# Performance work log

Measured on AMD Instinct MI355X. Metric: run time of the kernel, lower is better.

Reference implementation:

```python
import jax, jax.numpy as jnp
import numpy as np

N, D, C, G, NNZ = 256, 1024, 50000, 4, 300000
EPS = 1e-5


def setup_inputs() -> dict:
    key = jax.random.key(0)
    ks = jax.random.split(key, 5)
    return {
        "output": jax.random.normal(ks[0], (N, D), jnp.float32),
        "wt2_w": jax.random.normal(ks[1], (C, D), jnp.float32) * 0.02,
        "wt2_b": jnp.zeros((C,), jnp.float32),
        "A_vals": jax.random.uniform(ks[2], (G, NNZ), dtype=jnp.float32),
        "vec": jnp.ones((G,), jnp.float32),
        "A_rows": jax.random.randint(ks[3], (G, NNZ), 0, C, jnp.int32),
        "A_cols": jax.random.randint(ks[4], (G, NNZ), 0, C, jnp.int32),
    }


def reference(output, wt2_w, wt2_b, A_vals, vec, A_rows, A_cols):
    # BatchNorm1d(embed_dim, affine=False), training-mode batch stats (biased var)
    mean = jnp.mean(output, axis=0)
    var = jnp.var(output, axis=0)
    h0 = (output - mean) * jax.lax.rsqrt(var + EPS)
    # wt2 linear + swish -> Z [N, C]
    h1 = h0 @ wt2_w.T + wt2_b
    Z = h1 * jax.nn.sigmoid(h1)
    # multi-graph sparse propagation: neighbors += spmm(A_i * vec[i], Z^T)^T
    # spmm out[b, r] = sum_{e: rows[e]==r} vals[e] * Z[b, cols[e]]
    Zt = Z.T  # [C, N]
    neighbors = jnp.zeros_like(Z)
    n_graphs = A_vals.shape[0]
    for i in range(n_graphs):  # small fixed number of relation graphs
        vals = A_vals[i] * vec[i]               # learnable per-graph weight
        msgs = Zt[A_cols[i]] * vals[:, None]    # [nnz, N] gathered messages
        agg = jax.ops.segment_sum(msgs, A_rows[i], num_segments=Zt.shape[0])  # [C, N]
        neighbors = neighbors + agg.T
    # residual combine
    return neighbors + Z
```

## Files before the change

### kernel.cpp

```cpp
#include <hip/hip_runtime.h>

typedef __attribute__((ext_vector_type(8))) short short8;
typedef __attribute__((ext_vector_type(4))) float floatx4;

#define C_DIM 50000
#define D_DIM 1024
#define N_DIM 256
#define G_NUM 4
#define NNZ_G 300000
#define E_TOT (G_NUM * NNZ_G)

#define O_SB   0u
#define O_H0   8192u
#define O_ZT   532480u
#define O_CNT  26132480u
#define O_OFF  26332544u
#define O_CUR  26532608u
#define O_BS   26732672u
#define O_EDG  26733696u

static __device__ __forceinline__ unsigned short f2bf(float f) {
    union { float f; unsigned u; } v; v.f = f;
    unsigned r = v.u + 0x7fffu + ((v.u >> 16) & 1u);
    return (unsigned short)(r >> 16);
}
static __device__ __forceinline__ float bf2f(unsigned short u) {
    union { unsigned u; float f; } v; v.u = ((unsigned)u) << 16;
    return v.f;
}

__global__ __launch_bounds__(256) void k_bnstats(const float* __restrict__ x,
                                                 float* __restrict__ scale,
                                                 float* __restrict__ bias) {
    int d = blockIdx.x * 256 + threadIdx.x;
    float s = 0.f, ss = 0.f;
    for (int n = 0; n < N_DIM; ++n) {
        float v = x[n * D_DIM + d];
        s += v; ss += v * v;
    }
    float mean = s * (1.f / N_DIM);
    float var  = ss * (1.f / N_DIM) - mean * mean;
    float sc = rsqrtf(var + 1e-5f);
    scale[d] = sc;
    bias[d] = -mean * sc;
}

__global__ __launch_bounds__(256) void k_h0(const float* __restrict__ x,
                                            const float* __restrict__ scale,
                                            const float* __restrict__ bias,
                                            unsigned short* __restrict__ h0) {
    int id = blockIdx.x * 256 + threadIdx.x;
    int d = id & (D_DIM - 1);
    h0[id] = f2bf(x[id] * scale[d] + bias[d]);
}

__global__ __launch_bounds__(256) void k_gemm(const float* __restrict__ W,
                                              const float* __restrict__ wb,
                                              const unsigned short* __restrict__ h0,
                                              unsigned short* __restrict__ Zt) {
    __shared__ unsigned short As[64 * 40];
    __shared__ unsigned short Bs[256 * 40];
    const int t = threadIdx.x;
    const int c0 = blockIdx.x * 64;
    const int w = t >> 6, lane = t & 63;
    const int m = lane & 15, g = lane >> 4;
    const int arow = t >> 2, aseg = t & 3;

    floatx4 acc[4][4];
#pragma unroll
    for (int i = 0; i < 4; ++i)
#pragma unroll
        for (int j = 0; j < 4; ++j) acc[i][j] = (floatx4)0.f;

    for (int kk = 0; kk < D_DIM; kk += 32) {
        {
            int c = c0 + arow;
            float4 f0, f1;
            if (c < C_DIM) {
                const float4* src = (const float4*)&W[(size_t)c * D_DIM + kk + aseg * 8];
                f0 = src[0]; f1 = src[1];
            } else {
                f0 = f1 = make_float4(0.f, 0.f, 0.f, 0.f);
            }
            unsigned p0 = (unsigned)f2bf(f0.x) | ((unsigned)f2bf(f0.y) << 16);
            unsigned p1 = (unsigned)f2bf(f0.z) | ((unsigned)f2bf(f0.w) << 16);
            unsigned p2 = (unsigned)f2bf(f1.x) | ((unsigned)f2bf(f1.y) << 16);
            unsigned p3 = (unsigned)f2bf(f1.z) | ((unsigned)f2bf(f1.w) << 16);
            *(uint4*)&As[arow * 40 + aseg * 8] = make_uint4(p0, p1, p2, p3);
        }
        {
            const uint4* src = (const uint4*)&h0[(size_t)t * D_DIM + kk];
            uint4* dst = (uint4*)&Bs[t * 40];
            dst[0] = src[0]; dst[1] = src[1]; dst[2] = src[2]; dst[3] = src[3];
        }
        __syncthreads();

        short8 af[4], bfr[4];
#pragma unroll
        for (int i = 0; i < 4; ++i)
            af[i] = *(const short8*)&As[(i * 16 + m) * 40 + g * 8];
#pragma unroll
        for (int j = 0; j < 4; ++j)
            bfr[j] = *(const short8*)&Bs[(w * 64 + j * 16 + m) * 40 + g * 8];
#pragma unroll
        for (int i = 0; i < 4; ++i)
#pragma unroll
            for (int j = 0; j < 4; ++j)
                acc[i][j] = __builtin_amdgcn_mfma_f32_16x16x32_bf16(af[i], bfr[j], acc[i][j], 0, 0, 0);
        __syncthreads();
    }

#pragma unroll
    for (int i = 0; i < 4; ++i) {
#pragma unroll
        for (int j = 0; j < 4; ++j) {
            int b = w * 64 + j * 16 + m;
#pragma unroll
            for (int rr = 0; rr < 4; ++rr) {
                int c = c0 + i * 16 + g * 4 + rr;
                if (c < C_DIM) {
                    float x = acc[i][j][rr] + wb[c];
                    float z = x / (1.f + __expf(-x));
                    Zt[(size_t)c * 256 + b] = f2bf(z);
                }
            }
        }
    }
}

__global__ __launch_bounds__(256) void k_count(const int* __restrict__ rows,
                                               int* __restrict__ counts) {
    int id = blockIdx.x * 256 + threadIdx.x;
    if (id < E_TOT) atomicAdd(&counts[rows[id]], 1);
}

__global__ __launch_bounds__(256) void k_scan1(const int* __restrict__ counts,
                                               int* __restrict__ offsets,
                                               int* __restrict__ bsums) {
    __shared__ int sm[256];
    int t = threadIdx.x, i = blockIdx.x * 256 + t;
    int v = (i < C_DIM) ? counts[i] : 0;
    sm[t] = v; __syncthreads();
    for (int off = 1; off < 256; off <<= 1) {
        int x = (t >= off) ? sm[t - off] : 0;
        __syncthreads();
        sm[t] += x;
        __syncthreads();
    }
    if (i < C_DIM) offsets[i] = sm[t] - v;
    if (t == 255) bsums[blockIdx.x] = sm[255];
}

__global__ __launch_bounds__(256) void k_scan2(int* __restrict__ bsums,
                                               int* __restrict__ offsets) {
    __shared__ int sm[256];
    int t = threadIdx.x;
    int v = (t < 196) ? bsums[t] : 0;
    sm[t] = v; __syncthreads();
    for (int off = 1; off < 256; off <<= 1) {
        int x = (t >= off) ? sm[t - off] : 0;
        __syncthreads();
        sm[t] += x;
        __syncthreads();
    }
    if (t < 196) bsums[t] = sm[t] - v;
    if (t == 0) offsets[C_DIM] = sm[255];
}

__global__ __launch_bounds__(256) void k_scan3(const int* __restrict__ bsums,
                                               int* __restrict__ offsets,
                                               int* __restrict__ cursor) {
    int i = blockIdx.x * 256 + threadIdx.x;
    if (i < C_DIM) {
        int off = offsets[i] + bsums[blockIdx.x];
        offsets[i] = off;
        cursor[i] = off;
    }
}

__global__ __launch_bounds__(256) void k_scatter(const int* __restrict__ rows,
                                                 const int* __restrict__ cols,
                                                 const float* __restrict__ vals,
                                                 const float* __restrict__ vec,
                                                 int* __restrict__ cursor,
                                                 int2* __restrict__ edges) {
    int id = blockIdx.x * 256 + threadIdx.x;
    if (id < E_TOT) {
        int gidx = id / NNZ_G;
        float v = vals[id] * vec[gidx];
        int r = rows[id];
        int c = cols[id];
        int pos = atomicAdd(&cursor[r], 1);
        edges[pos] = make_int2(c, __float_as_int(v));
    }
}

__global__ __launch_bounds__(256) void k_agg(const unsigned short* __restrict__ Zt,
                                             const int* __restrict__ offsets,
                                             const int2* __restrict__ edges,
                                             float* __restrict__ out) {
    __shared__ float sm[32 * 256];
    const int t = threadIdx.x;
    const int w = t >> 6, lane = t & 63;
    const int r0 = blockIdx.x * 32;
    const int base = lane * 4;

#pragma unroll 1
    for (int k = 0; k < 8; ++k) {
        int lrow = w * 8 + k;
        int r = __builtin_amdgcn_readfirstlane(r0 + lrow);
        if (r < C_DIM) {
            ushort4 z = *(const ushort4*)&Zt[(size_t)r * 256 + base];
            float a0 = bf2f(z.x), a1 = bf2f(z.y), a2 = bf2f(z.z), a3 = bf2f(z.w);
            int s = offsets[r], e = offsets[r + 1];
            for (; s + 4 <= e; s += 4) {
                int2 e0 = edges[s], e1 = edges[s + 1], e2 = edges[s + 2], e3 = edges[s + 3];
                ushort4 g0 = *(const ushort4*)&Zt[(size_t)e0.x * 256 + base];
                ushort4 g1 = *(const ushort4*)&Zt[(size_t)e1.x * 256 + base];
                ushort4 g2 = *(const ushort4*)&Zt[(size_t)e2.x * 256 + base];
                ushort4 g3 = *(const ushort4*)&Zt[(size_t)e3.x * 256 + base];
                float v0 = __int_as_float(e0.y), v1 = __int_as_float(e1.y);
                float v2 = __int_as_float(e2.y), v3 = __int_as_float(e3.y);
                a0 += v0 * bf2f(g0.x) + v1 * bf2f(g1.x) + v2 * bf2f(g2.x) + v3 * bf2f(g3.x);
                a1 += v0 * bf2f(g0.y) + v1 * bf2f(g1.y) + v2 * bf2f(g2.y) + v3 * bf2f(g3.y);
                a2 += v0 * bf2f(g0.z) + v1 * bf2f(g1.z) + v2 * bf2f(g2.z) + v3 * bf2f(g3.z);
                a3 += v0 * bf2f(g0.w) + v1 * bf2f(g1.w) + v2 * bf2f(g2.w) + v3 * bf2f(g3.w);
            }
            for (; s < e; ++s) {
                int2 e0 = edges[s];
                ushort4 g0 = *(const ushort4*)&Zt[(size_t)e0.x * 256 + base];
                float v0 = __int_as_float(e0.y);
                a0 += v0 * bf2f(g0.x);
                a1 += v0 * bf2f(g0.y);
                a2 += v0 * bf2f(g0.z);
                a3 += v0 * bf2f(g0.w);
            }
            *(float4*)&sm[lrow * 256 + base] = make_float4(a0, a1, a2, a3);
        }
    }
    __syncthreads();

    int rows = C_DIM - r0; if (rows > 32) rows = 32;
    int nq = rows >> 2;
    float4* op = (float4*)&out[(size_t)t * C_DIM + r0];
#pragma unroll 1
    for (int q = 0; q < nq; ++q) {
        float4 o;
        o.x = sm[(q * 4 + 0) * 256 + t];
        o.y = sm[(q * 4 + 1) * 256 + t];
        o.z = sm[(q * 4 + 2) * 256 + t];
        o.w = sm[(q * 4 + 3) * 256 + t];
        op[q] = o;
    }
}

extern "C" void kernel_launch(void* const* d_in, const int* in_sizes, int n_in,
                              void* d_out, int out_size, void* d_ws, size_t ws_size,
                              hipStream_t stream) {
    (void)in_sizes; (void)n_in; (void)out_size; (void)ws_size;
    const float* x     = (const float*)d_in[0];
    const float* W     = (const float*)d_in[1];
    const float* wb    = (const float*)d_in[2];
    const float* Avals = (const float*)d_in[3];
    const float* vec   = (const float*)d_in[4];
    const int*   Arows = (const int*)d_in[5];
    const int*   Acols = (const int*)d_in[6];
    float* out = (float*)d_out;
    char* ws = (char*)d_ws;

    float* scale = (float*)(ws + O_SB);
    float* bias  = scale + 1024;
    unsigned short* h0 = (unsigned short*)(ws + O_H0);
    unsigned short* Zt = (unsigned short*)(ws + O_ZT);
    int* counts  = (int*)(ws + O_CNT);
    int* offsets = (int*)(ws + O_OFF);
    int* cursor  = (int*)(ws + O_CUR);
    int* bsums   = (int*)(ws + O_BS);
    int2* edges  = (int2*)(ws + O_EDG);

    hipMemsetAsync(counts, 0, C_DIM * sizeof(int), stream);

    k_bnstats<<<4, 256, 0, stream>>>(x, scale, bias);
    k_h0<<<1024, 256, 0, stream>>>(x, scale, bias, h0);
    k_count<<<(E_TOT + 255) / 256, 256, 0, stream>>>(Arows, counts);
    k_gemm<<<(C_DIM + 63) / 64, 256, 0, stream>>>(W, wb, h0, Zt);
    k_scan1<<<196, 256, 0, stream>>>(counts, offsets, bsums);
    k_scan2<<<1, 256, 0, stream>>>(bsums, offsets);
    k_scan3<<<196, 256, 0, stream>>>(bsums, offsets, cursor);
    k_scatter<<<(E_TOT + 255) / 256, 256, 0, stream>>>(Arows, Acols, Avals, vec, cursor, edges);
    k_agg<<<(C_DIM + 31) / 32, 256, 0, stream>>>(Zt, offsets, edges, out);
}
```

Baseline: 662.2 us.

## Double-buffer GEMM weight tiles and split aggregation across batch slices

The GEMM now keeps the bf16 weight tile in a double-buffered shared-memory array with a 64-wide K step and prefetches the next fp32 weight chunk into registers while MFMAs run. h0 operands are read straight from global memory instead of being staged in LDS, which removes one barrier per step. The aggregation kernel now splits the 256 batch columns into 8 slices per block and assigns 8 edges per wavefront in parallel, reducing with cross-lane shuffles, to raise memory-level parallelism on the gather. The cost is redundant reads of the edge and offset arrays across slices, plus smaller 32-float output rows per slice.

Result: slower. 748.4 us (+13.0%).

```diff
diff --git a/kernel.cpp b/kernel.cpp
--- a/kernel.cpp
+++ b/kernel.cpp
@@ -28,6 +28,9 @@
     union { unsigned u; float f; } v; v.u = ((unsigned)u) << 16;
     return v.f;
 }
+static __device__ __forceinline__ unsigned packbf(float a, float b) {
+    return (unsigned)f2bf(a) | ((unsigned)f2bf(b) << 16);
+}
 
 __global__ __launch_bounds__(256) void k_bnstats(const float* __restrict__ x,
                                                  float* __restrict__ scale,
@@ -54,60 +57,76 @@
     h0[id] = f2bf(x[id] * scale[d] + bias[d]);
 }
 
-__global__ __launch_bounds__(256) void k_gemm(const float* __restrict__ W,
-                                              const float* __restrict__ wb,
-                                              const unsigned short* __restrict__ h0,
-                                              unsigned short* __restrict__ Zt) {
-    __shared__ unsigned short As[64 * 40];
-    __shared__ unsigned short Bs[256 * 40];
+#define AST 72
+__global__ __launch_bounds__(256, 3) void k_gemm(const float* __restrict__ W,
+                                                 const float* __restrict__ wb,
+                                                 const unsigned short* __restrict__ h0,
+                                                 unsigned short* __restrict__ Zt) {
+    __shared__ unsigned short As[2][64 * AST];
     const int t = threadIdx.x;
     const int c0 = blockIdx.x * 64;
     const int w = t >> 6, lane = t & 63;
     const int m = lane & 15, g = lane >> 4;
     const int arow = t >> 2, aseg = t & 3;
 
+    const int cA = c0 + arow;
+    const bool aval = (cA < C_DIM);
+    const float* wsrc = &W[(size_t)cA * D_DIM + aseg * 16];
+    unsigned short* asdst0 = &As[0][arow * AST + aseg * 16];
+    unsigned short* asdst1 = &As[1][arow * AST + aseg * 16];
+    const unsigned short* bbase = h0 + ((w * 64 + m) * D_DIM + g * 8);
+
     floatx4 acc[4][4];
 #pragma unroll
     for (int i = 0; i < 4; ++i)
 #pragma unroll
         for (int j = 0; j < 4; ++j) acc[i][j] = (floatx4)0.f;
 
-    for (int kk = 0; kk < D_DIM; kk += 32) {
-        {
-            int c = c0 + arow;
-            float4 f0, f1;
-            if (c < C_DIM) {
-                const float4* src = (const float4*)&W[(size_t)c * D_DIM + kk + aseg * 8];
-                f0 = src[0]; f1 = src[1];
-            } else {
-                f0 = f1 = make_float4(0.f, 0.f, 0.f, 0.f);
-            }
-            unsigned p0 = (unsigned)f2bf(f0.x) | ((unsigned)f2bf(f0.y) << 16);
-            unsigned p1 = (unsigned)f2bf(f0.z) | ((unsigned)f2bf(f0.w) << 16);
-            unsigned p2 = (unsigned)f2bf(f1.x) | ((unsigned)f2bf(f1.y) << 16);
-            unsigned p3 = (unsigned)f2bf(f1.z) | ((unsigned)f2bf(f1.w) << 16);
-            *(uint4*)&As[arow * 40 + aseg * 8] = make_uint4(p0, p1, p2, p3);
-        }
-        {
-            const uint4* src = (const uint4*)&h0[(size_t)t * D_DIM + kk];
-            uint4* dst = (uint4*)&Bs[t * 40];
-            dst[0] = src[0]; dst[1] = src[1]; dst[2] = src[2]; dst[3] = src[3];
-        }
-        __syncthreads();
-
-        short8 af[4], bfr[4];
-#pragma unroll
-        for (int i = 0; i < 4; ++i)
-            af[i] = *(const short8*)&As[(i * 16 + m) * 40 + g * 8];
-#pragma unroll
-        for (int j = 0; j < 4; ++j)
-            bfr[j] = *(const short8*)&Bs[(w * 64 + j * 16 + m) * 40 + g * 8];
-#pragma unroll
-        for (int i = 0; i < 4; ++i)
+    float4 pf[4];
+#pragma unroll
+    for (int q = 0; q < 4; ++q)
+        pf[q] = aval ? *(const float4*)(wsrc + q * 4) : make_float4(0.f, 0.f, 0.f, 0.f);
+    {
+        uint4 u0 = make_uint4(packbf(pf[0].x, pf[0].y), packbf(pf[0].z, pf[0].w),
+                              packbf(pf[1].x, pf[1].y), packbf(pf[1].z, pf[1].w));
+        uint4 u1 = make_uint4(packbf(pf[2].x, pf[2].y), packbf(pf[2].z, pf[2].w),
+                              packbf(pf[3].x, pf[3].y), packbf(pf[3].z, pf[3].w));
+        *(uint4*)asdst0 = u0; *(uint4*)(asdst0 + 8) = u1;
+    }
+    __syncthreads();
+
+    for (int s = 0; s < 16; ++s) {
+        if (s < 15 && aval) {
+#pragma unroll
+            for (int q = 0; q < 4; ++q)
+                pf[q] = *(const float4*)(wsrc + (s + 1) * 64 + q * 4);
+        }
+        const unsigned short* asrd = &As[s & 1][0];
+#pragma unroll
+        for (int ksub = 0; ksub < 2; ++ksub) {
+            const unsigned short* bp = bbase + s * 64 + ksub * 32;
+            short8 af[4], bfr[4];
 #pragma unroll
             for (int j = 0; j < 4; ++j)
-                acc[i][j] = __builtin_amdgcn_mfma_f32_16x16x32_bf16(af[i], bfr[j], acc[i][j], 0, 0, 0);
-        __syncthreads();
+                bfr[j] = *(const short8*)(bp + j * 16 * D_DIM);
+#pragma unroll
+            for (int i = 0; i < 4; ++i)
+                af[i] = *(const short8*)&asrd[(i * 16 + m) * AST + ksub * 32 + g * 8];
+#pragma unroll
+            for (int i = 0; i < 4; ++i)
+#pragma unroll
+                for (int j = 0; j < 4; ++j)
+                    acc[i][j] = __builtin_amdgcn_mfma_f32_16x16x32_bf16(af[i], bfr[j], acc[i][j], 0, 0, 0);
+        }
+        if (s < 15) {
+            unsigned short* dst = ((s + 1) & 1) ? asdst1 : asdst0;
+            uint4 u0 = make_uint4(packbf(pf[0].x, pf[0].y), packbf(pf[0].z, pf[0].w),
+                                  packbf(pf[1].x, pf[1].y), packbf(pf[1].z, pf[1].w));
+            uint4 u1 = make_uint4(packbf(pf[2].x, pf[2].y), packbf(pf[2].z, pf[2].w),
+                                  packbf(pf[3].x, pf[3].y), packbf(pf[3].z, pf[3].w));
+            *(uint4*)dst = u0; *(uint4*)(dst + 8) = u1;
+            __syncthreads();
+        }
     }
 
 #pragma unroll
@@ -195,62 +214,70 @@
     }
 }
 
-__global__ __launch_bounds__(256) void k_agg(const unsigned short* __restrict__ Zt,
-                                             const int* __restrict__ offsets,
-                                             const int2* __restrict__ edges,
-                                             float* __restrict__ out) {
-    __shared__ float sm[32 * 256];
-    const int t = threadIdx.x;
-    const int w = t >> 6, lane = t & 63;
-    const int r0 = blockIdx.x * 32;
-    const int base = lane * 4;
+#define AGG_ROWS 64
+__global__ __launch_bounds__(256, 8) void k_agg(const unsigned short* __restrict__ Zt,
+                                                const int* __restrict__ offsets,
+                                                const int2* __restrict__ edges,
+                                                float* __restrict__ out) {
+    __shared__ float sm[AGG_ROWS * 33];
+    const int t = threadIdx.x, w = t >> 6, lane = t & 63;
+    const int p = blockIdx.x & 7;
+    const int r0 = (blockIdx.x >> 3) * AGG_ROWS;
+    const int esub = lane >> 3;
+    const int bq = lane & 7;
+    const int bOff = p * 32 + bq * 4;
 
 #pragma unroll 1
-    for (int k = 0; k < 8; ++k) {
-        int lrow = w * 8 + k;
-        int r = __builtin_amdgcn_readfirstlane(r0 + lrow);
-        if (r < C_DIM) {
-            ushort4 z = *(const ushort4*)&Zt[(size_t)r * 256 + base];
-            float a0 = bf2f(z.x), a1 = bf2f(z.y), a2 = bf2f(z.z), a3 = bf2f(z.w);
-            int s = offsets[r], e = offsets[r + 1];
-            for (; s + 4 <= e; s += 4) {
-                int2 e0 = edges[s], e1 = edges[s + 1], e2 = edges[s + 2], e3 = edges[s + 3];
-                ushort4 g0 = *(const ushort4*)&Zt[(size_t)e0.x * 256 + base];
-                ushort4 g1 = *(const ushort4*)&Zt[(size_t)e1.x * 256 + base];
-                ushort4 g2 = *(const ushort4*)&Zt[(size_t)e2.x * 256 + base];
-                ushort4 g3 = *(const ushort4*)&Zt[(size_t)e3.x * 256 + base];
-                float v0 = __int_as_float(e0.y), v1 = __int_as_float(e1.y);
-                float v2 = __int_as_float(e2.y), v3 = __int_as_float(e3.y);
-                a0 += v0 * bf2f(g0.x) + v1 * bf2f(g1.x) + v2 * bf2f(g2.x) + v3 * bf2f(g3.x);
-                a1 += v0 * bf2f(g0.y) + v1 * bf2f(g1.y) + v2 * bf2f(g2.y) + v3 * bf2f(g3.y);
-                a2 += v0 * bf2f(g0.z) + v1 * bf2f(g1.z) + v2 * bf2f(g2.z) + v3 * bf2f(g3.z);
-                a3 += v0 * bf2f(g0.w) + v1 * bf2f(g1.w) + v2 * bf2f(g2.w) + v3 * bf2f(g3.w);
-            }
-            for (; s < e; ++s) {
-                int2 e0 = edges[s];
-                ushort4 g0 = *(const ushort4*)&Zt[(size_t)e0.x * 256 + base];
-                float v0 = __int_as_float(e0.y);
-                a0 += v0 * bf2f(g0.x);
-                a1 += v0 * bf2f(g0.y);
-                a2 += v0 * bf2f(g0.z);
-                a3 += v0 * bf2f(g0.w);
-            }
-            *(float4*)&sm[lrow * 256 + base] = make_float4(a0, a1, a2, a3);
+    for (int k = 0; k < 16; ++k) {
+        int lrow = w * 16 + k;
+        int r = r0 + lrow;
+        if (r >= C_DIM) break;
+        int s = offsets[r], e = offsets[r + 1];
+        float a0 = 0.f, a1 = 0.f, a2 = 0.f, a3 = 0.f;
+        for (; s < e; s += 8) {
+            int idx = s + esub;
+            bool ok = idx < e;
+            int2 ed = edges[ok ? idx : s];
+            float v = ok ? __int_as_float(ed.y) : 0.f;
+            uint2 gz = *(const uint2*)&Zt[(size_t)ed.x * 256 + bOff];
+            a0 += v * bf2f((unsigned short)(gz.x & 0xffffu));
+            a1 += v * bf2f((unsigned short)(gz.x >> 16));
+            a2 += v * bf2f((unsigned short)(gz.y & 0xffffu));
+            a3 += v * bf2f((unsigned short)(gz.y >> 16));
+        }
+#pragma unroll
+        for (int d = 8; d < 64; d <<= 1) {
+            a0 += __shfl_xor(a0, d, 64);
+            a1 += __shfl_xor(a1, d, 64);
+            a2 += __shfl_xor(a2, d, 64);
+            a3 += __shfl_xor(a3, d, 64);
+        }
+        if (esub == 0) {
+            uint2 rz = *(const uint2*)&Zt[(size_t)r * 256 + bOff];
+            a0 += bf2f((unsigned short)(rz.x & 0xffffu));
+            a1 += bf2f((unsigned short)(rz.x >> 16));
+            a2 += bf2f((unsigned short)(rz.y & 0xffffu));
+            a3 += bf2f((unsigned short)(rz.y >> 16));
+            float* sp = &sm[lrow * 33 + bq * 4];
+            sp[0] = a0; sp[1] = a1; sp[2] = a2; sp[3] = a3;
         }
     }
     __syncthreads();
 
-    int rows = C_DIM - r0; if (rows > 32) rows = 32;
-    int nq = rows >> 2;
-    float4* op = (float4*)&out[(size_t)t * C_DIM + r0];
-#pragma unroll 1
-    for (int q = 0; q < nq; ++q) {
-        float4 o;
-        o.x = sm[(q * 4 + 0) * 256 + t];
-        o.y = sm[(q * 4 + 1) * 256 + t];
-        o.z = sm[(q * 4 + 2) * 256 + t];
-        o.w = sm[(q * 4 + 3) * 256 + t];
-        op[q] = o;
+    const int rq = t & 15;
+    const int bl = t >> 4;
+#pragma unroll
+    for (int pass = 0; pass < 2; ++pass) {
+        int b = p * 32 + pass * 16 + bl;
+        int rbase = r0 + rq * 4;
+        if (rbase + 3 < C_DIM) {
+            float4 o;
+            o.x = sm[(rq * 4 + 0) * 33 + pass * 16 + bl];
+            o.y = sm[(rq * 4 + 1) * 33 + pass * 16 + bl];
+            o.z = sm[(rq * 4 + 2) * 33 + pass * 16 + bl];
+            o.w = sm[(rq * 4 + 3) * 33 + pass * 16 + bl];
+            *(float4*)&out[(size_t)b * C_DIM + rbase] = o;
+        }
     }
 }
 
@@ -288,5 +315,5 @@
     k_scan2<<<1, 256, 0, stream>>>(bsums, offsets);
     k_scan3<<<196, 256, 0, stream>>>(bsums, offsets, cursor);
     k_scatter<<<(E_TOT + 255) / 256, 256, 0, stream>>>(Arows, Acols, Avals, vec, cursor, edges);
-    k_agg<<<(C_DIM + 31) / 32, 256, 0, stream>>>(Zt, offsets, edges, out);
-}
+    k_agg<<<((C_DIM + AGG_ROWS - 1) / AGG_ROWS) * 8, 256, 0, stream>>>(Zt, offsets, edges, out);
+}
```

## Restructure GEMM with register-streamed B and double-buffered A; widen agg gathers

Applied to the files above, without the earlier changes.

The GEMM now uses 32-row C tiles and double-buffers the converted W tile in LDS with a K-step of 64. The h0 operand is streamed directly from global memory into registers with a one-step prefetch instead of being staged in LDS, which reduces LDS traffic and cuts the barriers per step to one, at the cost of repeated global reads of h0 per block. The aggregation kernel splits each wave into two halves that process alternate edges. Each lane gathers 16-byte chunks of 8 bf16 values, and the halves are combined with a cross-lane shuffle, giving more memory-level parallelism per row at the cost of some wasted masked loads.

Result: slower. 679.1 us (+2.6%).

```diff
diff --git a/kernel.cpp b/kernel.cpp
--- a/kernel.cpp
+++ b/kernel.cpp
@@ -28,6 +28,15 @@
     union { unsigned u; float f; } v; v.u = ((unsigned)u) << 16;
     return v.f;
 }
+static __device__ __forceinline__ unsigned packbf(float a, float b) {
+    return (unsigned)f2bf(a) | ((unsigned)f2bf(b) << 16);
+}
+static __device__ __forceinline__ float bflo(unsigned u) {
+    union { unsigned u; float f; } v; v.u = u << 16; return v.f;
+}
+static __device__ __forceinline__ float bfhi(unsigned u) {
+    union { unsigned u; float f; } v; v.u = u & 0xffff0000u; return v.f;
+}
 
 __global__ __launch_bounds__(256) void k_bnstats(const float* __restrict__ x,
                                                  float* __restrict__ scale,
@@ -54,64 +63,80 @@
     h0[id] = f2bf(x[id] * scale[d] + bias[d]);
 }
 
-__global__ __launch_bounds__(256) void k_gemm(const float* __restrict__ W,
-                                              const float* __restrict__ wb,
-                                              const unsigned short* __restrict__ h0,
-                                              unsigned short* __restrict__ Zt) {
-    __shared__ unsigned short As[64 * 40];
-    __shared__ unsigned short Bs[256 * 40];
+#define AST 72
+__global__ __launch_bounds__(256, 4) void k_gemm(const float* __restrict__ W,
+                                                 const float* __restrict__ wb,
+                                                 const unsigned short* __restrict__ h0,
+                                                 unsigned short* __restrict__ Zt) {
+    __shared__ unsigned short As[2][32 * AST];
     const int t = threadIdx.x;
-    const int c0 = blockIdx.x * 64;
+    const int c0 = blockIdx.x * 32;
     const int w = t >> 6, lane = t & 63;
     const int m = lane & 15, g = lane >> 4;
-    const int arow = t >> 2, aseg = t & 3;
-
-    floatx4 acc[4][4];
-#pragma unroll
-    for (int i = 0; i < 4; ++i)
+    const int arow = t >> 3, aseg = t & 7;
+
+    const int cA = c0 + arow;
+    const bool aval = (cA < C_DIM);
+    const float* wsrc = &W[(size_t)cA * D_DIM + aseg * 8];
+    unsigned short* asdst0 = &As[0][arow * AST + aseg * 8];
+    unsigned short* asdst1 = &As[1][arow * AST + aseg * 8];
+    const unsigned short* bbase = h0 + ((w * 64 + m) * D_DIM + g * 8);
+
+    floatx4 acc[2][4];
+#pragma unroll
+    for (int i = 0; i < 2; ++i)
 #pragma unroll
         for (int j = 0; j < 4; ++j) acc[i][j] = (floatx4)0.f;
 
-    for (int kk = 0; kk < D_DIM; kk += 32) {
-        {
-            int c = c0 + arow;
-            float4 f0, f1;
-            if (c < C_DIM) {
-                const float4* src = (const float4*)&W[(size_t)c * D_DIM + kk + aseg * 8];
-                f0 = src[0]; f1 = src[1];
-            } else {
-                f0 = f1 = make_float4(0.f, 0.f, 0.f, 0.f);
+    float4 pf0 = make_float4(0.f, 0.f, 0.f, 0.f), pf1 = pf0;
+    if (aval) { pf0 = *(const float4*)wsrc; pf1 = *(const float4*)(wsrc + 4); }
+    *(uint4*)asdst0 = make_uint4(packbf(pf0.x, pf0.y), packbf(pf0.z, pf0.w),
+                                 packbf(pf1.x, pf1.y), packbf(pf1.z, pf1.w));
+    __syncthreads();
+
+    short8 bnxt[4];
+#pragma unroll
+    for (int j = 0; j < 4; ++j)
+        bnxt[j] = *(const short8*)(bbase + j * 16 * D_DIM);
+
+    for (int s = 0; s < 16; ++s) {
+        if (s < 15 && aval) {
+            pf0 = *(const float4*)(wsrc + (s + 1) * 64);
+            pf1 = *(const float4*)(wsrc + (s + 1) * 64 + 4);
+        }
+        const unsigned short* asrd = &As[s & 1][0];
+#pragma unroll
+        for (int ksub = 0; ksub < 2; ++ksub) {
+            short8 bcur[4];
+#pragma unroll
+            for (int j = 0; j < 4; ++j) bcur[j] = bnxt[j];
+            int nk = s * 2 + ksub + 1;
+            if (nk < 32) {
+                const unsigned short* bp = bbase + (nk >> 1) * 64 + (nk & 1) * 32;
+#pragma unroll
+                for (int j = 0; j < 4; ++j)
+                    bnxt[j] = *(const short8*)(bp + j * 16 * D_DIM);
             }
-            unsigned p0 = (unsigned)f2bf(f0.x) | ((unsigned)f2bf(f0.y) << 16);
-            unsigned p1 = (unsigned)f2bf(f0.z) | ((unsigned)f2bf(f0.w) << 16);
-            unsigned p2 = (unsigned)f2bf(f1.x) | ((unsigned)f2bf(f1.y) << 16);
-            unsigned p3 = (unsigned)f2bf(f1.z) | ((unsigned)f2bf(f1.w) << 16);
-            *(uint4*)&As[arow * 40 + aseg * 8] = make_uint4(p0, p1, p2, p3);
-        }
-        {
-            const uint4* src = (const uint4*)&h0[(size_t)t * D_DIM + kk];
-            uint4* dst = (uint4*)&Bs[t * 40];
-            dst[0] = src[0]; dst[1] = src[1]; dst[2] = src[2]; dst[3] = src[3];
-        }
-        __syncthreads();
-
-        short8 af[4], bfr[4];
-#pragma unroll
-        for (int i = 0; i < 4; ++i)
-            af[i] = *(const short8*)&As[(i * 16 + m) * 40 + g * 8];
-#pragma unroll
-        for (int j = 0; j < 4; ++j)
-            bfr[j] = *(const short8*)&Bs[(w * 64 + j * 16 + m) * 40 + g * 8];
-#pragma unroll
-        for (int i = 0; i < 4; ++i)
-#pragma unroll
-            for (int j = 0; j < 4; ++j)
-                acc[i][j] = __builtin_amdgcn_mfma_f32_16x16x32_bf16(af[i], bfr[j], acc[i][j], 0, 0, 0);
-        __syncthreads();
-    }
-
-#pragma unroll
-    for (int i = 0; i < 4; ++i) {
+            short8 af[2];
+#pragma unroll
+            for (int i = 0; i < 2; ++i)
+                af[i] = *(const short8*)&asrd[(i * 16 + m) * AST + ksub * 32 + g * 8];
+#pragma unroll
+            for (int i = 0; i < 2; ++i)
+#pragma unroll
+                for (int j = 0; j < 4; ++j)
+                    acc[i][j] = __builtin_amdgcn_mfma_f32_16x16x32_bf16(af[i], bcur[j], acc[i][j], 0, 0, 0);
+        }
+        if (s < 15) {
+            unsigned short* dst = ((s + 1) & 1) ? asdst1 : asdst0;
+            *(uint4*)dst = make_uint4(packbf(pf0.x, pf0.y), packbf(pf0.z, pf0.w),
+                                      packbf(pf1.x, pf1.y), packbf(pf1.z, pf1.w));
+            __syncthreads();
+        }
+    }
+
+#pragma unroll
+    for (int i = 0; i < 2; ++i) {
 #pragma unroll
         for (int j = 0; j < 4; ++j) {
             int b = w * 64 + j * 16 + m;
@@ -203,39 +228,45 @@
     const int t = threadIdx.x;
     const int w = t >> 6, lane = t & 63;
     const int r0 = blockIdx.x * 32;
-    const int base = lane * 4;
+    const int h = lane >> 5;
+    const int b8 = lane & 31;
+    const int zoff = b8 * 8;
 
 #pragma unroll 1
     for (int k = 0; k < 8; ++k) {
         int lrow = w * 8 + k;
-        int r = __builtin_amdgcn_readfirstlane(r0 + lrow);
-        if (r < C_DIM) {
-            ushort4 z = *(const ushort4*)&Zt[(size_t)r * 256 + base];
-            float a0 = bf2f(z.x), a1 = bf2f(z.y), a2 = bf2f(z.z), a3 = bf2f(z.w);
-            int s = offsets[r], e = offsets[r + 1];
-            for (; s + 4 <= e; s += 4) {
-                int2 e0 = edges[s], e1 = edges[s + 1], e2 = edges[s + 2], e3 = edges[s + 3];
-                ushort4 g0 = *(const ushort4*)&Zt[(size_t)e0.x * 256 + base];
-                ushort4 g1 = *(const ushort4*)&Zt[(size_t)e1.x * 256 + base];
-                ushort4 g2 = *(const ushort4*)&Zt[(size_t)e2.x * 256 + base];
-                ushort4 g3 = *(const ushort4*)&Zt[(size_t)e3.x * 256 + base];
-                float v0 = __int_as_float(e0.y), v1 = __int_as_float(e1.y);
-                float v2 = __int_as_float(e2.y), v3 = __int_as_float(e3.y);
-                a0 += v0 * bf2f(g0.x) + v1 * bf2f(g1.x) + v2 * bf2f(g2.x) + v3 * bf2f(g3.x);
-                a1 += v0 * bf2f(g0.y) + v1 * bf2f(g1.y) + v2 * bf2f(g2.y) + v3 * bf2f(g3.y);
-                a2 += v0 * bf2f(g0.z) + v1 * bf2f(g1.z) + v2 * bf2f(g2.z) + v3 * bf2f(g3.z);
-                a3 += v0 * bf2f(g0.w) + v1 * bf2f(g1.w) + v2 * bf2f(g2.w) + v3 * bf2f(g3.w);
+        int r = r0 + lrow;
+        if (r >= C_DIM) break;
+        float a0 = 0.f, a1 = 0.f, a2 = 0.f, a3 = 0.f;
+        float a4 = 0.f, a5 = 0.f, a6 = 0.f, a7 = 0.f;
+        const int s0 = offsets[r], e0 = offsets[r + 1];
+        for (int s = s0; s < e0; s += 8) {
+#pragma unroll
+            for (int u = 0; u < 4; ++u) {
+                int idx = s + u * 2 + h;
+                bool ok = idx < e0;
+                int2 ed = edges[ok ? idx : s0];
+                float v = ok ? __int_as_float(ed.y) : 0.f;
+                uint4 gz = *(const uint4*)&Zt[(size_t)ed.x * 256 + zoff];
+                a0 += v * bflo(gz.x); a1 += v * bfhi(gz.x);
+                a2 += v * bflo(gz.y); a3 += v * bfhi(gz.y);
+                a4 += v * bflo(gz.z); a5 += v * bfhi(gz.z);
+                a6 += v * bflo(gz.w); a7 += v * bfhi(gz.w);
             }
-            for (; s < e; ++s) {
-                int2 e0 = edges[s];
-                ushort4 g0 = *(const ushort4*)&Zt[(size_t)e0.x * 256 + base];
-                float v0 = __int_as_float(e0.y);
-                a0 += v0 * bf2f(g0.x);
-                a1 += v0 * bf2f(g0.y);
-                a2 += v0 * bf2f(g0.z);
-                a3 += v0 * bf2f(g0.w);
-            }
-            *(float4*)&sm[lrow * 256 + base] = make_float4(a0, a1, a2, a3);
+        }
+        a0 += __shfl_xor(a0, 32, 64); a1 += __shfl_xor(a1, 32, 64);
+        a2 += __shfl_xor(a2, 32, 64); a3 += __shfl_xor(a3, 32, 64);
+        a4 += __shfl_xor(a4, 32, 64); a5 += __shfl_xor(a5, 32, 64);
+        a6 += __shfl_xor(a6, 32, 64); a7 += __shfl_xor(a7, 32, 64);
+        if (h == 0) {
+            uint4 rz = *(const uint4*)&Zt[(size_t)r * 256 + zoff];
+            a0 += bflo(rz.x); a1 += bfhi(rz.x);
+            a2 += bflo(rz.y); a3 += bfhi(rz.y);
+            a4 += bflo(rz.z); a5 += bfhi(rz.z);
+            a6 += bflo(rz.w); a7 += bfhi(rz.w);
+            float* sp = &sm[lrow * 256 + zoff];
+            *(float4*)sp = make_float4(a0, a1, a2, a3);
+            *(float4*)(sp + 4) = make_float4(a4, a5, a6, a7);
         }
     }
     __syncthreads();
@@ -283,7 +314,7 @@
     k_bnstats<<<4, 256, 0, stream>>>(x, scale, bias);
     k_h0<<<1024, 256, 0, stream>>>(x, scale, bias, h0);
     k_count<<<(E_TOT + 255) / 256, 256, 0, stream>>>(Arows, counts);
-    k_gemm<<<(C_DIM + 63) / 64, 256, 0, stream>>>(W, wb, h0, Zt);
+    k_gemm<<<(C_DIM + 31) / 32, 256, 0, stream>>>(W, wb, h0, Zt);
     k_scan1<<<196, 256, 0, stream>>>(counts, offsets, bsums);
     k_scan2<<<1, 256, 0, stream>>>(bsums, offsets);
     k_scan3<<<196, 256, 0, stream>>>(bsums, offsets, cursor);
```
